# Optimization experiments

Hardware: AMD Instinct MI355X
Metric: run time of the kernel (lower is better)

## Reference

```python
import jax, jax.numpy as jnp
import numpy as np
from jax import lax

N, DEG, D_IN, D_FEAT, D_HID, D_REP, G = 32768, 16, 128, 256, 256, 128, 64


def setup_inputs() -> dict:
    key = jax.random.key(0)
    ks = jax.random.split(key, 24)
    def w(k, shape):
        return (jax.random.normal(k, shape, jnp.float32) / np.sqrt(shape[0])).astype(jnp.float32)
    inp = {
        "in_feat": jax.random.normal(ks[0], (N, D_IN), jnp.float32),
        "neighbors": jax.random.randint(ks[1], (N, DEG), 0, N, jnp.int32),
        "node2graph": jnp.sort(jax.random.randint(ks[2], (N,), 0, G, jnp.int32)),
        # layer 1 (SAGEConv 128 -> 256, lstm aggregator: LSTM(128,128))
        "w_ih1": w(ks[3], (4 * D_IN, D_IN)),
        "w_hh1": w(ks[4], (4 * D_IN, D_IN)),
        "b_lstm1": jnp.zeros((4 * D_IN,), jnp.float32),
        "w_self1": w(ks[5], (D_IN, D_FEAT)),
        "w_neigh1": w(ks[6], (D_IN, D_FEAT)),
        "b1": jnp.zeros((D_FEAT,), jnp.float32),
        # layer 2 (SAGEConv 256 -> 256, LSTM(256,256))
        "w_ih2": w(ks[7], (4 * D_FEAT, D_FEAT)),
        "w_hh2": w(ks[8], (4 * D_FEAT, D_FEAT)),
        "b_lstm2": jnp.zeros((4 * D_FEAT,), jnp.float32),
        "w_self2": w(ks[9], (D_FEAT, D_HID)),
        "w_neigh2": w(ks[10], (D_FEAT, D_HID)),
        "b2": jnp.zeros((D_HID,), jnp.float32),
        # heads
        "w_mu": w(ks[11], (D_HID, D_REP)),
        "b_mu": jnp.zeros((D_REP,), jnp.float32),
        "w_sigma": w(ks[12], (D_HID, D_REP)),
        "b_sigma": jnp.zeros((D_REP,), jnp.float32),
    }
    return inp


def _lstm_agg(seq, w_ih, w_hh, b):
    # seq: [N, L, D] neighbor messages; LSTM with zero init, return final hidden h.
    n, _, d = seq.shape
    h0 = jnp.zeros((n, d), seq.dtype)
    def step(carry, x):
        h, c = carry
        gates = x @ w_ih.T + h @ w_hh.T + b  # [N, 4D]
        i, f, g, o = jnp.split(gates, 4, axis=-1)  # pytorch gate order i,f,g,o
        c = jax.nn.sigmoid(f) * c + jax.nn.sigmoid(i) * jnp.tanh(g)
        h = jax.nn.sigmoid(o) * jnp.tanh(c)
        return (h, c), None
    (h, _), _ = lax.scan(step, (h0, h0), jnp.swapaxes(seq, 0, 1))
    return h


def _sage_lstm(feat, neighbors, w_ih, w_hh, b_lstm, w_self, w_neigh, b):
    msgs = feat[neighbors]                      # irregular gather [N, DEG, D]
    h_n = _lstm_agg(msgs, w_ih, w_hh, b_lstm)   # [N, D]
    return feat @ w_self + h_n @ w_neigh + b


def reference(in_feat, neighbors, node2graph,
              w_ih1, w_hh1, b_lstm1, w_self1, w_neigh1, b1,
              w_ih2, w_hh2, b_lstm2, w_self2, w_neigh2, b2,
              w_mu, b_mu, w_sigma, b_sigma):
    h = _sage_lstm(in_feat, neighbors, w_ih1, w_hh1, b_lstm1, w_self1, w_neigh1, b1)
    h = jax.nn.relu(h)
    h = _sage_lstm(h, neighbors, w_ih2, w_hh2, b_lstm2, w_self2, w_neigh2, b2)
    # dgl.mean_nodes: per-graph mean over nodes
    sums = jax.ops.segment_sum(h, node2graph, num_segments=G)
    cnts = jax.ops.segment_sum(jnp.ones((h.shape[0],), h.dtype), node2graph, num_segments=G)
    x = sums / jnp.maximum(cnts, 1.0)[:, None]
    return (x @ w_mu + b_mu, x @ w_sigma + b_sigma)
```

## Files before the change

kernel.cpp:

```cpp
#include <hip/hip_runtime.h>
#include <hip/hip_bf16.h>
#include <cstddef>

#define NN_   32768
#define DEG_  16
#define D1_   128
#define D2_   256
#define G_    64
#define DREP_ 128

typedef __attribute__((ext_vector_type(8))) short bf16x8;
typedef __attribute__((ext_vector_type(4))) float f32x4;
typedef __attribute__((ext_vector_type(4))) unsigned short us4;
typedef unsigned short ushort_t;

__device__ __attribute__((aligned(16))) ushort_t g_feat1[(size_t)NN_ * D1_];
__device__ __attribute__((aligned(16))) ushort_t g_hfeat[(size_t)NN_ * D2_];
__device__ __attribute__((aligned(16))) ushort_t g_hA[(size_t)NN_ * D2_];
__device__ __attribute__((aligned(16))) ushort_t g_hB[(size_t)NN_ * D2_];
__device__ __attribute__((aligned(16))) ushort_t g_c[(size_t)NN_ * D2_];
__device__ __attribute__((aligned(16))) ushort_t g_P[(size_t)NN_ * 1024];
__device__ __attribute__((aligned(16))) float    g_outh[(size_t)NN_ * D2_];
__device__ __attribute__((aligned(16))) ushort_t g_wih1[512 * 128];
__device__ __attribute__((aligned(16))) ushort_t g_whh1[512 * 128];
__device__ __attribute__((aligned(16))) ushort_t g_wself1[256 * 128];
__device__ __attribute__((aligned(16))) ushort_t g_wneigh1[256 * 128];
__device__ __attribute__((aligned(16))) ushort_t g_wih2[1024 * 256];
__device__ __attribute__((aligned(16))) ushort_t g_whh2[1024 * 256];
__device__ __attribute__((aligned(16))) ushort_t g_wself2[256 * 256];
__device__ __attribute__((aligned(16))) ushort_t g_wneigh2[256 * 256];
__device__ float g_gsum[G_ * D2_];
__device__ int   g_gcnt[G_];

__device__ __forceinline__ ushort_t f2bf(float f) {
    unsigned int u = __float_as_uint(f);
    u += 0x7fffu + ((u >> 16) & 1u);
    return (ushort_t)(u >> 16);
}
__device__ __forceinline__ float bf2f(ushort_t u) {
    return __uint_as_float(((unsigned int)u) << 16);
}
__device__ __forceinline__ float sigf(float x) { return 1.f / (1.f + __expf(-x)); }
__device__ __forceinline__ float tanhf_(float x) { return 1.f - 2.f / (__expf(2.f * x) + 1.f); }

__global__ __launch_bounds__(256) void cvt_bf16(const float* __restrict__ src,
                                                ushort_t* __restrict__ dst, int n)
{
    int i = blockIdx.x * 256 + threadIdx.x;
    if (i < n) dst[i] = f2bf(src[i]);
}

__global__ __launch_bounds__(256) void cvt_bf16_T(const float* __restrict__ src,
                                                  ushort_t* __restrict__ dst, int K, int N)
{
    int i = blockIdx.x * 256 + threadIdx.x;
    if (i < K * N) {
        int k = i / N, n = i % N;
        dst[n * K + k] = f2bf(src[i]);
    }
}

template<bool DUAL, bool HAS_BIAS, bool RELU, bool OUTBF>
__global__ __launch_bounds__(256) void gemm_mfma(
    const ushort_t* __restrict__ A1, const ushort_t* __restrict__ B1,
    const ushort_t* __restrict__ A2, const ushort_t* __restrict__ B2,
    const float* __restrict__ bias, float* __restrict__ Cf,
    ushort_t* __restrict__ Cb, int M, int N, int K)
{
    __shared__ ushort_t As[64][72];
    __shared__ ushort_t Bs[64][72];
    const int tid = threadIdx.x;
    const int l = tid & 63, w = tid >> 6;
    const int m0 = blockIdx.y * 64, n0 = blockIdx.x * 64;

    f32x4 acc[4];
#pragma unroll
    for (int m = 0; m < 4; ++m) acc[m] = (f32x4){0.f, 0.f, 0.f, 0.f};

    const int npass = DUAL ? 2 : 1;
    for (int pass = 0; pass < npass; ++pass) {
        const ushort_t* __restrict__ A = (DUAL && pass) ? A2 : A1;
        const ushort_t* __restrict__ B = (DUAL && pass) ? B2 : B1;
        for (int k0 = 0; k0 < K; k0 += 64) {
#pragma unroll
            for (int i = 0; i < 2; ++i) {
                int cid = tid + 256 * i;
                int row = cid >> 3, col = (cid & 7) * 8;
                *(uint4*)&As[row][col] = *(const uint4*)&A[(size_t)(m0 + row) * K + k0 + col];
                *(uint4*)&Bs[row][col] = *(const uint4*)&B[(size_t)(n0 + row) * K + k0 + col];
            }
            __syncthreads();
#pragma unroll
            for (int kk = 0; kk < 64; kk += 32) {
                bf16x8 b = *(const bf16x8*)&Bs[16 * w + (l & 15)][kk + (l >> 4) * 8];
#pragma unroll
                for (int m = 0; m < 4; ++m) {
                    bf16x8 a = *(const bf16x8*)&As[16 * m + (l & 15)][kk + (l >> 4) * 8];
                    acc[m] = __builtin_amdgcn_mfma_f32_16x16x32_bf16(a, b, acc[m], 0, 0, 0);
                }
            }
            __syncthreads();
        }
    }

#pragma unroll
    for (int m = 0; m < 4; ++m) {
#pragma unroll
        for (int r = 0; r < 4; ++r) {
            int row = m0 + 16 * m + (l >> 4) * 4 + r;
            int col = n0 + 16 * w + (l & 15);
            float v = acc[m][r];
            if (HAS_BIAS) v += bias[col];
            if (RELU) v = fmaxf(v, 0.f);
            if (OUTBF) Cb[(size_t)row * N + col] = f2bf(v);
            else       Cf[(size_t)row * N + col] = v;
        }
    }
}

template<int D>
__global__ __launch_bounds__(256, 2) void lstm_step3(
    const ushort_t* __restrict__ h_prev, const ushort_t* __restrict__ whh,
    const ushort_t* __restrict__ P, const int* __restrict__ nbr,
    ushort_t* __restrict__ c, ushort_t* __restrict__ h_next, int t)
{
    constexpr int HP = D + 8;
    constexpr int KC = D / 32;
    constexpr int NT = 8;
    __shared__ ushort_t As[128][HP];

    const int tid = threadIdx.x;
    const int l = tid & 63, w = tid >> 6;
    const int lr = l & 15, lg = l >> 4;
    const int m0 = blockIdx.x * 128;
    const int d0 = blockIdx.y * 64;
    const int dd = d0 + w * 16 + lg * 4;

    constexpr int CH = 128 * D / 8;
#pragma unroll
    for (int cid = tid; cid < CH; cid += 256) {
        int row = cid / (D / 8), cc = (cid % (D / 8)) * 8;
        *(uint4*)&As[row][cc] = *(const uint4*)&h_prev[(size_t)(m0 + row) * D + cc];
    }

    f32x4 acc[4][NT];
#pragma unroll
    for (int g = 0; g < 4; ++g)
#pragma unroll
        for (int nt = 0; nt < NT; ++nt) acc[g][nt] = (f32x4){0.f, 0.f, 0.f, 0.f};

    __syncthreads();

    const ushort_t* __restrict__ wbase = &whh[(size_t)(d0 + w * 16 + lr) * D + lg * 8];
    bf16x8 a_cur[4], a_nxt[4];
#pragma unroll
    for (int g = 0; g < 4; ++g)
        a_cur[g] = *(const bf16x8*)&wbase[(size_t)g * D * D];

#pragma unroll
    for (int kc = 0; kc < KC; ++kc) {
        if (kc + 1 < KC) {
#pragma unroll
            for (int g = 0; g < 4; ++g)
                a_nxt[g] = *(const bf16x8*)&wbase[(size_t)g * D * D + (kc + 1) * 32];
        }
        bf16x8 b[NT];
#pragma unroll
        for (int nt = 0; nt < NT; ++nt)
            b[nt] = *(const bf16x8*)&As[nt * 16 + lr][kc * 32 + lg * 8];
#pragma unroll
        for (int g = 0; g < 4; ++g)
#pragma unroll
            for (int nt = 0; nt < NT; ++nt)
                acc[g][nt] = __builtin_amdgcn_mfma_f32_16x16x32_bf16(
                    a_cur[g], b[nt], acc[g][nt], 0, 0, 0);
#pragma unroll
        for (int g = 0; g < 4; ++g) a_cur[g] = a_nxt[g];
    }

#pragma unroll
    for (int nt = 0; nt < NT; ++nt) {
        const int node = m0 + nt * 16 + lr;
        const int j = nbr[(size_t)node * DEG_ + t];
        const size_t base = (size_t)j * (4 * D) + dd;
        us4 pg[4];
#pragma unroll
        for (int g = 0; g < 4; ++g)
            pg[g] = *(const us4*)&P[base + g * D];
        const size_t ci = (size_t)node * D + dd;
        us4 cold = *(const us4*)&c[ci];

        us4 cnew, hnew;
#pragma unroll
        for (int r = 0; r < 4; ++r) {
            float gi = acc[0][nt][r] + bf2f(pg[0][r]);
            float gf = acc[1][nt][r] + bf2f(pg[1][r]);
            float gg = acc[2][nt][r] + bf2f(pg[2][r]);
            float go = acc[3][nt][r] + bf2f(pg[3][r]);
            float cn = sigf(gf) * bf2f(cold[r]) + sigf(gi) * tanhf_(gg);
            cnew[r] = f2bf(cn);
            hnew[r] = f2bf(sigf(go) * tanhf_(cn));
        }
        *(us4*)&c[ci] = cnew;
        *(us4*)&h_next[ci] = hnew;
    }
}

template<int D>
__global__ __launch_bounds__(256) void cell_first(
    const ushort_t* __restrict__ P, const int* __restrict__ nbr,
    ushort_t* __restrict__ c, ushort_t* __restrict__ h_out)
{
    int idx = blockIdx.x * 256 + threadIdx.x;
    int n = idx / D, d = idx % D;
    int j = nbr[n * DEG_];
    size_t base = (size_t)j * (4 * D);
    float gi = bf2f(P[base + d]);
    float gg = bf2f(P[base + 2 * D + d]);
    float go = bf2f(P[base + 3 * D + d]);
    float cn = sigf(gi) * tanhf_(gg);
    c[idx] = f2bf(cn);
    h_out[idx] = f2bf(sigf(go) * tanhf_(cn));
}

__global__ void graph_counts(const int* __restrict__ n2g, int* __restrict__ cnt)
{
    __shared__ int lb[G_ + 1];
    int g = threadIdx.x;
    if (g <= G_) {
        int lo = 0, hi = NN_;
        while (lo < hi) {
            int mid = (lo + hi) >> 1;
            if (n2g[mid] < g) lo = mid + 1; else hi = mid;
        }
        lb[g] = lo;
    }
    __syncthreads();
    if (g < G_) cnt[g] = lb[g + 1] - lb[g];
}

__global__ __launch_bounds__(256) void seg_sum(
    const float* __restrict__ X, const int* __restrict__ n2g,
    float* __restrict__ gsum)
{
    int d = threadIdx.x;
    int n_start = blockIdx.x * 64;
    int cur = n2g[n_start];
    float acc = 0.f;
    for (int n = n_start; n < n_start + 64; ++n) {
        int g = n2g[n];
        if (g != cur) {
            atomicAdd(&gsum[cur * D2_ + d], acc);
            acc = 0.f;
            cur = g;
        }
        acc += X[(size_t)n * D2_ + d];
    }
    atomicAdd(&gsum[cur * D2_ + d], acc);
}

__global__ __launch_bounds__(128) void head_kernel(
    const float* __restrict__ gsum, const int* __restrict__ cnt,
    const float* __restrict__ w_mu, const float* __restrict__ b_mu,
    const float* __restrict__ w_sig, const float* __restrict__ b_sig,
    float* __restrict__ out)
{
    __shared__ float x[D2_];
    int g = blockIdx.x, j = threadIdx.x;
    float inv = 1.f / fmaxf((float)cnt[g], 1.f);
    x[j] = gsum[g * D2_ + j] * inv;
    x[j + 128] = gsum[g * D2_ + 128 + j] * inv;
    __syncthreads();
    float mu = b_mu[j], sg = b_sig[j];
    for (int k = 0; k < D2_; ++k) {
        float xv = x[k];
        mu += xv * w_mu[k * DREP_ + j];
        sg += xv * w_sig[k * DREP_ + j];
    }
    out[g * DREP_ + j] = mu;
    out[G_ * DREP_ + g * DREP_ + j] = sg;
}

extern "C" void kernel_launch(void* const* d_in, const int* in_sizes, int n_in,
                              void* d_out, int out_size, void* d_ws, size_t ws_size,
                              hipStream_t stream)
{
    const float* in_feat   = (const float*)d_in[0];
    const int*   neighbors = (const int*)d_in[1];
    const int*   node2graph= (const int*)d_in[2];
    const float* w_ih1     = (const float*)d_in[3];
    const float* w_hh1     = (const float*)d_in[4];
    const float* b_lstm1   = (const float*)d_in[5];
    const float* w_self1   = (const float*)d_in[6];
    const float* w_neigh1  = (const float*)d_in[7];
    const float* b1        = (const float*)d_in[8];
    const float* w_ih2     = (const float*)d_in[9];
    const float* w_hh2     = (const float*)d_in[10];
    const float* b_lstm2   = (const float*)d_in[11];
    const float* w_self2   = (const float*)d_in[12];
    const float* w_neigh2  = (const float*)d_in[13];
    const float* b2        = (const float*)d_in[14];
    const float* w_mu      = (const float*)d_in[15];
    const float* b_mu      = (const float*)d_in[16];
    const float* w_sigma   = (const float*)d_in[17];
    const float* b_sigma   = (const float*)d_in[18];

    void *pF1, *pHF, *pHA, *pHB, *pC, *pP, *pOH;
    void *pWI1, *pWH1, *pWS1, *pWN1, *pWI2, *pWH2, *pWS2, *pWN2, *pGS, *pGC;
    hipGetSymbolAddress(&pF1, HIP_SYMBOL(g_feat1));
    hipGetSymbolAddress(&pHF, HIP_SYMBOL(g_hfeat));
    hipGetSymbolAddress(&pHA, HIP_SYMBOL(g_hA));
    hipGetSymbolAddress(&pHB, HIP_SYMBOL(g_hB));
    hipGetSymbolAddress(&pC,  HIP_SYMBOL(g_c));
    hipGetSymbolAddress(&pP,  HIP_SYMBOL(g_P));
    hipGetSymbolAddress(&pOH, HIP_SYMBOL(g_outh));
    hipGetSymbolAddress(&pWI1, HIP_SYMBOL(g_wih1));
    hipGetSymbolAddress(&pWH1, HIP_SYMBOL(g_whh1));
    hipGetSymbolAddress(&pWS1, HIP_SYMBOL(g_wself1));
    hipGetSymbolAddress(&pWN1, HIP_SYMBOL(g_wneigh1));
    hipGetSymbolAddress(&pWI2, HIP_SYMBOL(g_wih2));
    hipGetSymbolAddress(&pWH2, HIP_SYMBOL(g_whh2));
    hipGetSymbolAddress(&pWS2, HIP_SYMBOL(g_wself2));
    hipGetSymbolAddress(&pWN2, HIP_SYMBOL(g_wneigh2));
    hipGetSymbolAddress(&pGS, HIP_SYMBOL(g_gsum));
    hipGetSymbolAddress(&pGC, HIP_SYMBOL(g_gcnt));

    ushort_t* feat1 = (ushort_t*)pF1;
    ushort_t* hfeat = (ushort_t*)pHF;
    ushort_t* hA    = (ushort_t*)pHA;
    ushort_t* hB    = (ushort_t*)pHB;
    ushort_t* c     = (ushort_t*)pC;
    ushort_t* P     = (ushort_t*)pP;
    float*    outh  = (float*)pOH;
    ushort_t* wih1  = (ushort_t*)pWI1;
    ushort_t* whh1  = (ushort_t*)pWH1;
    ushort_t* wself1= (ushort_t*)pWS1;
    ushort_t* wneigh1=(ushort_t*)pWN1;
    ushort_t* wih2  = (ushort_t*)pWI2;
    ushort_t* whh2  = (ushort_t*)pWH2;
    ushort_t* wself2= (ushort_t*)pWS2;
    ushort_t* wneigh2=(ushort_t*)pWN2;
    float*    gsum  = (float*)pGS;
    int*      gcnt  = (int*)pGC;

    cvt_bf16<<<(NN_ * D1_ + 255) / 256, 256, 0, stream>>>(in_feat, feat1, NN_ * D1_);
    cvt_bf16<<<(512 * 128 + 255) / 256, 256, 0, stream>>>(w_ih1, wih1, 512 * 128);
    cvt_bf16<<<(512 * 128 + 255) / 256, 256, 0, stream>>>(w_hh1, whh1, 512 * 128);
    cvt_bf16_T<<<(128 * 256 + 255) / 256, 256, 0, stream>>>(w_self1, wself1, 128, 256);
    cvt_bf16_T<<<(128 * 256 + 255) / 256, 256, 0, stream>>>(w_neigh1, wneigh1, 128, 256);
    cvt_bf16<<<(1024 * 256 + 255) / 256, 256, 0, stream>>>(w_ih2, wih2, 1024 * 256);
    cvt_bf16<<<(1024 * 256 + 255) / 256, 256, 0, stream>>>(w_hh2, whh2, 1024 * 256);
    cvt_bf16_T<<<(256 * 256 + 255) / 256, 256, 0, stream>>>(w_self2, wself2, 256, 256);
    cvt_bf16_T<<<(256 * 256 + 255) / 256, 256, 0, stream>>>(w_neigh2, wneigh2, 256, 256);

    gemm_mfma<false, true, false, true>
        <<<dim3(512 / 64, NN_ / 64), 256, 0, stream>>>(
            feat1, wih1, nullptr, nullptr, b_lstm1, nullptr, P, NN_, 512, D1_);

    cell_first<D1_><<<(NN_ * D1_) / 256, 256, 0, stream>>>(P, neighbors, c, hA);
    for (int t = 1; t < DEG_; ++t) {
        const ushort_t* hp = (t & 1) ? hA : hB;
        ushort_t*       hn = (t & 1) ? hB : hA;
        lstm_step3<D1_><<<dim3(NN_ / 128, D1_ / 64), 256, 0, stream>>>(
            hp, whh1, P, neighbors, c, hn, t);
    }

    gemm_mfma<true, true, true, true>
        <<<dim3(256 / 64, NN_ / 64), 256, 0, stream>>>(
            feat1, wself1, hB, wneigh1, b1, nullptr, hfeat, NN_, D2_, D1_);

    gemm_mfma<false, true, false, true>
        <<<dim3(1024 / 64, NN_ / 64), 256, 0, stream>>>(
            hfeat, wih2, nullptr, nullptr, b_lstm2, nullptr, P, NN_, 1024, D2_);

    cell_first<D2_><<<(NN_ * D2_) / 256, 256, 0, stream>>>(P, neighbors, c, hA);
    for (int t = 1; t < DEG_; ++t) {
        const ushort_t* hp = (t & 1) ? hA : hB;
        ushort_t*       hn = (t & 1) ? hB : hA;
        lstm_step3<D2_><<<dim3(NN_ / 128, D2_ / 64), 256, 0, stream>>>(
            hp, whh2, P, neighbors, c, hn, t);
    }

    gemm_mfma<true, true, false, false>
        <<<dim3(256 / 64, NN_ / 64), 256, 0, stream>>>(
            hfeat, wself2, hB, wneigh2, b2, outh, nullptr, NN_, D2_, D2_);

    hipMemsetAsync(gsum, 0, (size_t)G_ * D2_ * sizeof(float), stream);
    graph_counts<<<1, 128, 0, stream>>>(node2graph, gcnt);
    seg_sum<<<NN_ / 64, 256, 0, stream>>>(outh, node2graph, gsum);
    head_kernel<<<G_, 128, 0, stream>>>(gsum, gcnt, w_mu, b_mu, w_sigma, b_sigma,
                                        (float*)d_out);
}
```

Baseline: 1.465 ms.

## Split LSTM step tile across 8 waves to halve per-wave accumulators

The recurrent LSTM step kernel now runs 512 threads per block, with two groups of four waves each handling half of the 128 node rows. Each wave holds only 4 node tiles of accumulators instead of 8, and the register double-buffering of the weight fragments is dropped in favour of loading them per k-chunk. The goal is lower register pressure and more waves resident per CU to hide the gather and LDS latency. In exchange, each weight fragment is now loaded by twice as many waves, and latency hiding relies on occupancy rather than explicit prefetch.

```diff
diff --git a/kernel.cpp b/kernel.cpp
--- a/kernel.cpp
+++ b/kernel.cpp
@@ -119,26 +119,28 @@
 }
 
 template<int D>
-__global__ __launch_bounds__(256, 2) void lstm_step3(
+__global__ __launch_bounds__(512, 4) void lstm_step4(
     const ushort_t* __restrict__ h_prev, const ushort_t* __restrict__ whh,
     const ushort_t* __restrict__ P, const int* __restrict__ nbr,
     ushort_t* __restrict__ c, ushort_t* __restrict__ h_next, int t)
 {
     constexpr int HP = D + 8;
     constexpr int KC = D / 32;
-    constexpr int NT = 8;
+    constexpr int NT = 4;
     __shared__ ushort_t As[128][HP];
 
     const int tid = threadIdx.x;
     const int l = tid & 63, w = tid >> 6;
     const int lr = l & 15, lg = l >> 4;
+    const int mh = w >> 2;
+    const int wd = w & 3;
     const int m0 = blockIdx.x * 128;
     const int d0 = blockIdx.y * 64;
-    const int dd = d0 + w * 16 + lg * 4;
+    const int dd = d0 + wd * 16 + lg * 4;
 
     constexpr int CH = 128 * D / 8;
 #pragma unroll
-    for (int cid = tid; cid < CH; cid += 256) {
+    for (int cid = tid; cid < CH; cid += 512) {
         int row = cid / (D / 8), cc = (cid % (D / 8)) * 8;
         *(uint4*)&As[row][cc] = *(const uint4*)&h_prev[(size_t)(m0 + row) * D + cc];
     }
@@ -151,36 +153,26 @@
 
     __syncthreads();
 
-    const ushort_t* __restrict__ wbase = &whh[(size_t)(d0 + w * 16 + lr) * D + lg * 8];
-    bf16x8 a_cur[4], a_nxt[4];
-#pragma unroll
-    for (int g = 0; g < 4; ++g)
-        a_cur[g] = *(const bf16x8*)&wbase[(size_t)g * D * D];
-
+    const ushort_t* __restrict__ wbase = &whh[(size_t)(d0 + wd * 16 + lr) * D + lg * 8];
 #pragma unroll
     for (int kc = 0; kc < KC; ++kc) {
-        if (kc + 1 < KC) {
+        bf16x8 a[4];
+#pragma unroll
+        for (int g = 0; g < 4; ++g)
+            a[g] = *(const bf16x8*)&wbase[(size_t)g * D * D + kc * 32];
+#pragma unroll
+        for (int nt = 0; nt < NT; ++nt) {
+            bf16x8 b = *(const bf16x8*)&As[mh * 64 + nt * 16 + lr][kc * 32 + lg * 8];
 #pragma unroll
             for (int g = 0; g < 4; ++g)
-                a_nxt[g] = *(const bf16x8*)&wbase[(size_t)g * D * D + (kc + 1) * 32];
-        }
-        bf16x8 b[NT];
-#pragma unroll
-        for (int nt = 0; nt < NT; ++nt)
-            b[nt] = *(const bf16x8*)&As[nt * 16 + lr][kc * 32 + lg * 8];
-#pragma unroll
-        for (int g = 0; g < 4; ++g)
-#pragma unroll
-            for (int nt = 0; nt < NT; ++nt)
                 acc[g][nt] = __builtin_amdgcn_mfma_f32_16x16x32_bf16(
-                    a_cur[g], b[nt], acc[g][nt], 0, 0, 0);
-#pragma unroll
-        for (int g = 0; g < 4; ++g) a_cur[g] = a_nxt[g];
+                    a[g], b, acc[g][nt], 0, 0, 0);
+        }
     }
 
 #pragma unroll
     for (int nt = 0; nt < NT; ++nt) {
-        const int node = m0 + nt * 16 + lr;
+        const int node = m0 + mh * 64 + nt * 16 + lr;
         const int j = nbr[(size_t)node * DEG_ + t];
         const size_t base = (size_t)j * (4 * D) + dd;
         us4 pg[4];
@@ -361,7 +353,7 @@
     for (int t = 1; t < DEG_; ++t) {
         const ushort_t* hp = (t & 1) ? hA : hB;
         ushort_t*       hn = (t & 1) ? hB : hA;
-        lstm_step3<D1_><<<dim3(NN_ / 128, D1_ / 64), 256, 0, stream>>>(
+        lstm_step4<D1_><<<dim3(NN_ / 128, D1_ / 64), 512, 0, stream>>>(
             hp, whh1, P, neighbors, c, hn, t);
     }
 
@@ -377,7 +369,7 @@
     for (int t = 1; t < DEG_; ++t) {
         const ushort_t* hp = (t & 1) ? hA : hB;
         ushort_t*       hn = (t & 1) ? hB : hA;
-        lstm_step3<D2_><<<dim3(NN_ / 128, D2_ / 64), 256, 0, stream>>>(
+        lstm_step4<D2_><<<dim3(NN_ / 128, D2_ / 64), 512, 0, stream>>>(
             hp, whh2, P, neighbors, c, hn, t);
     }
 
```

Measured after the change: 1.659 ms. 1.13x slower.
